# Kernel tuning notes

Measured on AMD Instinct MI355X. Metric: run time of the kernel, lower is better.

Reference implementation:

```python
import jax, jax.numpy as jnp
import numpy as np

N = 50000      # nodes
E = 800000     # edges
CIN = 128
CH = 128
COUT = 64
EPS = 1e-5     # BatchNorm eps


def setup_inputs() -> dict:
    key = jax.random.key(0)
    ks = jax.random.split(key, 16)
    s = 0.1  # weight scale for numerical stability
    return {
        "x": jax.random.normal(ks[0], (N, CIN), jnp.float32),
        "edge_index": jax.random.randint(ks[1], (2, E), 0, N, jnp.int32),
        "edge_weights": jax.random.uniform(ks[2], (E,), jnp.float32),
        "w1": jax.random.normal(ks[3], (CIN, CH), jnp.float32) * s,
        "b1": jnp.zeros((CH,), jnp.float32),
        "bn1_g": jnp.ones((CH,), jnp.float32),
        "bn1_b": jnp.zeros((CH,), jnp.float32),
        "bn1_m": jax.random.normal(ks[4], (CH,), jnp.float32) * 0.1,
        "bn1_v": jax.random.uniform(ks[5], (CH,), jnp.float32) + 0.5,
        "conv_ws": jax.random.normal(ks[6], (2, CH, CH), jnp.float32) * s,
        "conv_bs": jnp.zeros((2, CH), jnp.float32),
        "bns_g": jnp.ones((2, CH), jnp.float32),
        "bns_b": jnp.zeros((2, CH), jnp.float32),
        "bns_m": jax.random.normal(ks[7], (2, CH), jnp.float32) * 0.1,
        "bns_v": jax.random.uniform(ks[8], (2, CH), jnp.float32) + 0.5,
        "lin1_w": jax.random.normal(ks[9], (CH, CH), jnp.float32) * s,
        "lin1_b": jnp.zeros((CH,), jnp.float32),
        "lin2_w": jax.random.normal(ks[10], (CH, COUT), jnp.float32) * s,
        "lin2_b": jnp.zeros((COUT,), jnp.float32),
    }


def _bn(h, g, b, m, v):
    # BatchNorm1d in eval mode: running statistics
    return (h - m) * jax.lax.rsqrt(v + EPS) * g + b


def _gcn(h, w, b, src, dst, norm, n):
    # GCNConv: out[dst] += norm_e * (h @ W)[src]  (self loops already in src/dst)
    h = h @ w
    msg = h[src] * norm[:, None]                 # [E+N, CH]
    return jax.ops.segment_sum(msg, dst, num_segments=n) + b


def reference(x, edge_index, edge_weights, w1, b1, bn1_g, bn1_b, bn1_m, bn1_v,
              conv_ws, conv_bs, bns_g, bns_b, bns_m, bns_v,
              lin1_w, lin1_b, lin2_w, lin2_b):
    n = x.shape[0]
    loop = jnp.arange(n, dtype=edge_index.dtype)
    src = jnp.concatenate([edge_index[0], loop])
    dst = jnp.concatenate([edge_index[1], loop])
    ew = jnp.concatenate([edge_weights, jnp.ones((n,), edge_weights.dtype)])
    # symmetric degree normalization (PyG gcn_norm)
    deg = jax.ops.segment_sum(ew, dst, num_segments=n)
    dis = jnp.where(deg > 0, jax.lax.rsqrt(deg), 0.0)
    norm = dis[src] * ew * dis[dst]

    lrelu = jax.nn.leaky_relu  # slope 0.01, matches F.leaky_relu default
    h = lrelu(_bn(_gcn(x, w1, b1, src, dst, norm, n), bn1_g, bn1_b, bn1_m, bn1_v))
    for i in range(conv_ws.shape[0]):
        h = lrelu(_bn(_gcn(h, conv_ws[i], conv_bs[i], src, dst, norm, n),
                      bns_g[i], bns_b[i], bns_m[i], bns_v[i]) + h)
    h = lrelu(h @ lin1_w + lin1_b)
    # dropout is identity in eval mode
    return h @ lin2_w + lin2_b
```

## Files before the change

kernel.cpp:

```cpp
#include <hip/hip_runtime.h>
#include <hip/hip_bf16.h>


constexpr int   NN    = 50000;
constexpr int   EE    = 800000;
constexpr int   CH    = 128;
constexpr int   SLOTS = 64;
constexpr int   NBUK  = 782;
constexpr int   RCAP  = 2048;
constexpr int   EPB   = 2048;
constexpr float EPS   = 1e-5f;

typedef __attribute__((ext_vector_type(8))) short bf16x8;
typedef __attribute__((ext_vector_type(4))) float f32x4;
typedef unsigned long long u64;
typedef unsigned short u16;

__device__ inline u16 f2bf_rne(float f) {
  unsigned u = __float_as_uint(f);
  unsigned r = u + 0x7fffu + ((u >> 16) & 1u);
  return (u16)(r >> 16);
}
__device__ inline float bf2f(unsigned h16) {
  return __uint_as_float(h16 << 16);
}


__global__ __launch_bounds__(256) void bin_kernel(const int* __restrict__ ei,
                                                  const float* __restrict__ ew,
                                                  unsigned* __restrict__ gcur,
                                                  u64* __restrict__ bins) {
  __shared__ unsigned cnt[NBUK];
  __shared__ unsigned base[NBUK];
  const int tid = threadIdx.x;
  for (int b = tid; b < NBUK; b += 256) cnt[b] = 0;
  __syncthreads();
  const int e0 = blockIdx.x * EPB;
  unsigned pk[8]; u16 bkt[8]; u16 rnk[8]; unsigned char dl[8];
  #pragma unroll
  for (int i = 0; i < 8; i++) {
    int e = e0 + i * 256 + tid;
    if (e < EE) {
      int s = ei[e], d = ei[EE + e];
      float w = ew[e];
      bkt[i] = (u16)(d >> 6);
      dl[i]  = (unsigned char)(d & 63);
      pk[i]  = ((unsigned)f2bf_rne(w) << 16) | (unsigned)s;
      rnk[i] = (u16)atomicAdd(&cnt[bkt[i]], 1u);
    } else bkt[i] = 0xffffu;
  }
  __syncthreads();
  for (int b = tid; b < NBUK; b += 256) {
    unsigned c = cnt[b];
    base[b] = c ? atomicAdd(&gcur[b * 16], c) : 0u;
  }
  __syncthreads();
  #pragma unroll
  for (int i = 0; i < 8; i++) {
    if (bkt[i] == 0xffffu) continue;
    unsigned pos = base[bkt[i]] + rnk[i];
    if (pos < RCAP)
      bins[(size_t)bkt[i] * RCAP + pos] = ((u64)dl[i] << 32) | pk[i];
  }
}


__global__ __launch_bounds__(256) void scatter_kernel(const unsigned* __restrict__ gcur,
                                                      const u64* __restrict__ bins,
                                                      unsigned* __restrict__ ell,
                                                      float* __restrict__ dis) {
  __shared__ unsigned rank[64];
  __shared__ float    wsum[64];
  const int b   = blockIdx.x;
  const int tid = threadIdx.x;
  if (tid < 64) { rank[tid] = 1u; wsum[tid] = 0.f; }
  __syncthreads();
  unsigned cnt = gcur[b * 16];
  if (cnt > RCAP) cnt = RCAP;
  const u64* src = bins + (size_t)b * RCAP;
  for (unsigned i = tid; i < cnt; i += 256) {
    u64 v = src[i];
    unsigned pk = (unsigned)v;
    unsigned dl = (unsigned)(v >> 32);
    unsigned r = atomicAdd(&rank[dl], 1u);
    if (r < SLOTS)
      ell[((size_t)(b * 64 + dl)) * SLOTS + r] = pk;
    atomicAdd(&wsum[dl], bf2f(pk >> 16));
  }
  __syncthreads();
  if (tid < 64) {
    int node = b * 64 + tid;
    if (node < NN) {
      unsigned c = rank[tid];
      if (c > SLOTS) c = SLOTS;
      ell[(size_t)node * SLOTS] = c;
      dis[node] = rsqrtf(1.0f + wsum[tid]);
    }
  }
}

constexpr int NB_WZ = (73728 + 384 + 255) / 256;

__global__ void wswz_kernel(
    const float* __restrict__ w1, const float* __restrict__ bn1_g, const float* __restrict__ bn1_v,
    const float* __restrict__ conv_ws, const float* __restrict__ bns_g, const float* __restrict__ bns_v,
    const float* __restrict__ lin1_w, const float* __restrict__ lin2_w,
    const float* __restrict__ b1, const float* __restrict__ bn1_b, const float* __restrict__ bn1_m,
    const float* __restrict__ conv_bs, const float* __restrict__ bns_b, const float* __restrict__ bns_m,
    u16* __restrict__ w1h, u16* __restrict__ w1l,
    u16* __restrict__ c0h, u16* __restrict__ c0l,
    u16* __restrict__ c1h, u16* __restrict__ c1l,
    u16* __restrict__ l1h, u16* __restrict__ l1l,
    u16* __restrict__ l2h, u16* __restrict__ l2l,
    float* __restrict__ beff)
{
  int idx = blockIdx.x * 256 + threadIdx.x;
  if (idx >= 73728) {
    int r = idx - 73728;
    if (r >= 384) return;
    int l = r >> 7, c = r & 127;
    float bc, gg, bb, mm, vv;
    if (l == 0) { bc = b1[c]; gg = bn1_g[c]; bb = bn1_b[c]; mm = bn1_m[c]; vv = bn1_v[c]; }
    else {
      int o = (l - 1) * 128 + c;
      bc = conv_bs[o]; gg = bns_g[o]; bb = bns_b[o]; mm = bns_m[o]; vv = bns_v[o];
    }
    beff[r] = (bc - mm) * gg * rsqrtf(vv + EPS) + bb;
    return;
  }
  const float* W; const float* g = nullptr; const float* v = nullptr;
  u16 *hi, *lo; int CO = 128; int local;
  if      (idx < 16384) { W = w1;              g = bn1_g;     v = bn1_v;     hi = w1h; lo = w1l; local = idx; }
  else if (idx < 32768) { W = conv_ws;         g = bns_g;     v = bns_v;     hi = c0h; lo = c0l; local = idx - 16384; }
  else if (idx < 49152) { W = conv_ws + 16384; g = bns_g+128; v = bns_v+128; hi = c1h; lo = c1l; local = idx - 32768; }
  else if (idx < 65536) { W = lin1_w;                                        hi = l1h; lo = l1l; local = idx - 49152; }
  else                  { W = lin2_w;                                        hi = l2h; lo = l2l; local = idx - 65536; CO = 64; }
  int k = local / CO, n = local % CO;
  float w = W[local];
  if (g) w *= g[n] * rsqrtf(v[n] + EPS);
  int NCT = CO / 16;
  int kchunk = k >> 5, kin = k & 31, quad = kin >> 3, j = kin & 7;
  int ct = n >> 4, l = (quad << 4) | (n & 15);
  size_t pos = ((size_t)(kchunk * NCT + ct) * 64 + l) * 8 + j;
  u16 h = f2bf_rne(w);
  hi[pos] = h;
  lo[pos] = f2bf_rne(w - bf2f(h));
}

__global__ __launch_bounds__(256) void gemm1_kernel(
    const float* __restrict__ Ain,
    const u16* __restrict__ Whi, const u16* __restrict__ Wlo,
    const float* __restrict__ dis, u16* __restrict__ Cout)
{
  __shared__ float lds[64][CH + 4];
  const int tid  = threadIdx.x;
  const int wave = tid >> 6;
  const int lane = tid & 63;
  const int quad = lane >> 4;
  const int mrow = lane & 15;
  const int row0 = blockIdx.x * 64;

  int arow = row0 + wave * 16 + mrow;
  if (arow >= NN) arow = NN - 1;

  bf16x8 ahi[4], alo[4];
  const float* Ar = Ain + (size_t)arow * CH;
  #pragma unroll
  for (int c = 0; c < 4; c++) {
    int off = c * 32 + quad * 8;
    float4 f0 = *(const float4*)(Ar + off);
    float4 f1 = *(const float4*)(Ar + off + 4);
    float f[8] = {f0.x, f0.y, f0.z, f0.w, f1.x, f1.y, f1.z, f1.w};
    #pragma unroll
    for (int j = 0; j < 8; j++) {
      u16 h = f2bf_rne(f[j]);
      ahi[c][j] = (short)h;
      alo[c][j] = (short)f2bf_rne(f[j] - bf2f(h));
    }
  }

  f32x4 acc[8];
  #pragma unroll
  for (int t = 0; t < 8; t++) acc[t] = (f32x4){0.f, 0.f, 0.f, 0.f};
  #pragma unroll
  for (int c = 0; c < 4; c++) {
    #pragma unroll
    for (int t = 0; t < 8; t++) {
      size_t base = ((size_t)(c * 8 + t) * 64 + lane) * 8;
      bf16x8 bh = *(const bf16x8*)(Whi + base);
      bf16x8 bl = *(const bf16x8*)(Wlo + base);
      acc[t] = __builtin_amdgcn_mfma_f32_16x16x32_bf16(ahi[c], bh, acc[t], 0, 0, 0);
      acc[t] = __builtin_amdgcn_mfma_f32_16x16x32_bf16(alo[c], bh, acc[t], 0, 0, 0);
      acc[t] = __builtin_amdgcn_mfma_f32_16x16x32_bf16(ahi[c], bl, acc[t], 0, 0, 0);
    }
  }

  #pragma unroll
  for (int t = 0; t < 8; t++)
    #pragma unroll
    for (int r = 0; r < 4; r++)
      lds[wave * 16 + quad * 4 + r][t * 16 + mrow] = acc[t][r];
  __syncthreads();

  #pragma unroll
  for (int i = tid; i < 64 * CH / 4; i += 256) {
    int row = (i * 4) / CH;
    int col = (i * 4) % CH;
    int grow = row0 + row;
    if (grow >= NN) continue;
    float rs = dis[grow];
    const float* lp = &lds[row][col];
    u16* cp = (u16*)Cout + (size_t)grow * CH + col;
    unsigned p0 = ((unsigned)f2bf_rne(lp[1] * rs) << 16) | f2bf_rne(lp[0] * rs);
    unsigned p1 = ((unsigned)f2bf_rne(lp[3] * rs) << 16) | f2bf_rne(lp[2] * rs);
    *(uint2*)cp = make_uint2(p0, p1);
  }
}

template<bool RES, bool WH>
__device__ __forceinline__ void gather4_qw(
    const u16* __restrict__ hwin, const unsigned* __restrict__ ell,
    const float* __restrict__ dis, const float* __restrict__ beff,
    const u16* __restrict__ res, u16* __restrict__ hout,
    unsigned* __restrict__ hsbase,
    int nbase, int lane, int sub, int grp)
{
  int nd0 = nbase < NN ? nbase : NN - 1;
  unsigned wcur = ell[(size_t)nd0 * SLOTS + lane];
  for (int r = 0; r < 4; r++) {
    int node = nbase + r;
    int nd = node < NN ? node : NN - 1;
    unsigned myword = wcur;
    if (r < 3) {
      int n2 = node + 1 < NN ? node + 1 : NN - 1;
      wcur = ell[(size_t)n2 * SLOTS + lane];
    }
    int cnt = __shfl((int)myword, 0);
    if (cnt > SLOTS) cnt = SLOTS;
    float a[8] = {0.f, 0.f, 0.f, 0.f, 0.f, 0.f, 0.f, 0.f};
    for (int j = 0; j < cnt; j += 16) {
      unsigned sidx[4]; float wv[4];
      #pragma unroll
      for (int q = 0; q < 4; q++) {
        int jj = j + q * 4 + grp;
        unsigned e = (unsigned)__shfl((int)myword, jj & 63);
        float    w = (jj == 0) ? 1.0f : bf2f(e >> 16);
        unsigned s = (jj == 0) ? (unsigned)nd : (e & 0xffffu);
        if (jj >= cnt) { w = 0.f; s = (unsigned)nd; }
        sidx[q] = s; wv[q] = w;
      }
      uint4 h[4];
      #pragma unroll
      for (int q = 0; q < 4; q++)
        h[q] = *(const uint4*)(hwin + (size_t)sidx[q] * CH + sub * 8);
      #pragma unroll
      for (int q = 0; q < 4; q++) {
        float w = wv[q];
        a[0] = fmaf(w, bf2f(h[q].x & 0xffffu), a[0]); a[1] = fmaf(w, bf2f(h[q].x >> 16), a[1]);
        a[2] = fmaf(w, bf2f(h[q].y & 0xffffu), a[2]); a[3] = fmaf(w, bf2f(h[q].y >> 16), a[3]);
        a[4] = fmaf(w, bf2f(h[q].z & 0xffffu), a[4]); a[5] = fmaf(w, bf2f(h[q].z >> 16), a[5]);
        a[6] = fmaf(w, bf2f(h[q].w & 0xffffu), a[6]); a[7] = fmaf(w, bf2f(h[q].w >> 16), a[7]);
      }
    }
    #pragma unroll
    for (int k = 0; k < 8; k++) {
      a[k] += __shfl_xor(a[k], 16);
      a[k] += __shfl_xor(a[k], 32);
    }
    if (grp == 0) {
      float disd = dis[nd];
      int c = sub * 8;
      float4 be0 = *(const float4*)(beff + c);
      float4 be1 = *(const float4*)(beff + c + 4);
      float y[8];
      y[0] = a[0] * disd + be0.x; y[1] = a[1] * disd + be0.y;
      y[2] = a[2] * disd + be0.z; y[3] = a[3] * disd + be0.w;
      y[4] = a[4] * disd + be1.x; y[5] = a[5] * disd + be1.y;
      y[6] = a[6] * disd + be1.z; y[7] = a[7] * disd + be1.w;
      if constexpr (RES) {
        uint4 rr = *(const uint4*)(res + (size_t)nd * CH + c);
        y[0] += bf2f(rr.x & 0xffffu); y[1] += bf2f(rr.x >> 16);
        y[2] += bf2f(rr.y & 0xffffu); y[3] += bf2f(rr.y >> 16);
        y[4] += bf2f(rr.z & 0xffffu); y[5] += bf2f(rr.z >> 16);
        y[6] += bf2f(rr.w & 0xffffu); y[7] += bf2f(rr.w >> 16);
      }
      #pragma unroll
      for (int k = 0; k < 8; k++) y[k] = y[k] > 0.f ? y[k] : 0.01f * y[k];
      uint4 o;
      o.x = ((unsigned)f2bf_rne(y[1]) << 16) | f2bf_rne(y[0]);
      o.y = ((unsigned)f2bf_rne(y[3]) << 16) | f2bf_rne(y[2]);
      o.z = ((unsigned)f2bf_rne(y[5]) << 16) | f2bf_rne(y[4]);
      o.w = ((unsigned)f2bf_rne(y[7]) << 16) | f2bf_rne(y[6]);
      if constexpr (WH) {
        if (node < NN) *(uint4*)(hout + (size_t)node * CH + c) = o;
      }
      *(uint4*)&hsbase[r * 68 + sub * 4] = o;
    }
  }
}

template<bool RES>
__global__ __launch_bounds__(256, 6) void fuse_kernel(
    const u16* __restrict__ hwin,
    const unsigned* __restrict__ ell, const float* __restrict__ dis,
    const float* __restrict__ beff, const u16* __restrict__ res,
    const u16* __restrict__ Whi, const u16* __restrict__ Wlo,
    u16* __restrict__ hout, u16* __restrict__ hwout)
{
  __shared__ unsigned hs[16][68];
  const int tid  = threadIdx.x;
  const int wave = tid >> 6;
  const int lane = tid & 63;
  const int sub  = lane & 15;
  const int grp  = lane >> 4;
  const int row0 = blockIdx.x * 16;

  gather4_qw<RES, true>(hwin, ell, dis, beff, res, hout,
                        &hs[wave * 4][0], row0 + wave * 4, lane, sub, grp);
  __syncthreads();

  bf16x8 af[4];
  #pragma unroll
  for (int c = 0; c < 4; c++)
    af[c] = *(const bf16x8*)&hs[sub][c * 16 + grp * 4];
  __syncthreads();

  f32x4 acc[2];
  #pragma unroll
  for (int t = 0; t < 2; t++) acc[t] = (f32x4){0.f, 0.f, 0.f, 0.f};
  #pragma unroll
  for (int c = 0; c < 4; c++) {
    #pragma unroll
    for (int t = 0; t < 2; t++) {
      size_t base = ((size_t)(c * 8 + wave * 2 + t) * 64 + lane) * 8;
      bf16x8 bh = *(const bf16x8*)(Whi + base);
      bf16x8 bl = *(const bf16x8*)(Wlo + base);
      acc[t] = __builtin_amdgcn_mfma_f32_16x16x32_bf16(af[c], bh, acc[t], 0, 0, 0);
      acc[t] = __builtin_amdgcn_mfma_f32_16x16x32_bf16(af[c], bl, acc[t], 0, 0, 0);
    }
  }

  u16* hs16 = (u16*)&hs[0][0];
  #pragma unroll
  for (int r = 0; r < 4; r++) {
    int row = grp * 4 + r;
    float rs = dis[row0 + row];
    #pragma unroll
    for (int t = 0; t < 2; t++)
      hs16[row * 136 + wave * 32 + t * 16 + sub] = f2bf_rne(acc[t][r] * rs);
  }
  __syncthreads();
  {
    int row   = tid >> 4;
    int chunk = tid & 15;
    uint4 o = *(const uint4*)(hs16 + row * 136 + chunk * 8);
    *(uint4*)(hwout + (size_t)(row0 + row) * CH + chunk * 8) = o;
  }
}

__global__ __launch_bounds__(256, 6) void fuse_last_kernel(
    const u16* __restrict__ hwin,
    const unsigned* __restrict__ ell, const float* __restrict__ dis,
    const float* __restrict__ beff, const u16* __restrict__ res,
    const u16* __restrict__ l1h, const u16* __restrict__ l1l,
    const float* __restrict__ b1,
    const u16* __restrict__ l2h, const u16* __restrict__ l2l,
    const float* __restrict__ b2, float* __restrict__ out)
{
  __shared__ unsigned hs[16][68];
  __shared__ float    fs[16][132];
  const int tid  = threadIdx.x;
  const int wave = tid >> 6;
  const int lane = tid & 63;
  const int sub  = lane & 15;
  const int grp  = lane >> 4;
  const int row0 = blockIdx.x * 16;

  gather4_qw<true, false>(hwin, ell, dis, beff, res, nullptr,
                          &hs[wave * 4][0], row0 + wave * 4, lane, sub, grp);
  __syncthreads();

  bf16x8 af[4];
  #pragma unroll
  for (int c = 0; c < 4; c++)
    af[c] = *(const bf16x8*)&hs[sub][c * 16 + grp * 4];

  f32x4 acc[2];
  #pragma unroll
  for (int t = 0; t < 2; t++) acc[t] = (f32x4){0.f, 0.f, 0.f, 0.f};
  #pragma unroll
  for (int c = 0; c < 4; c++) {
    #pragma unroll
    for (int t = 0; t < 2; t++) {
      size_t base = ((size_t)(c * 8 + wave * 2 + t) * 64 + lane) * 8;
      bf16x8 bh = *(const bf16x8*)(l1h + base);
      bf16x8 bl = *(const bf16x8*)(l1l + base);
      acc[t] = __builtin_amdgcn_mfma_f32_16x16x32_bf16(af[c], bh, acc[t], 0, 0, 0);
      acc[t] = __builtin_amdgcn_mfma_f32_16x16x32_bf16(af[c], bl, acc[t], 0, 0, 0);
    }
  }
  #pragma unroll
  for (int t = 0; t < 2; t++) {
    int col = wave * 32 + t * 16 + sub;
    float bb = b1[col];
    #pragma unroll
    for (int r = 0; r < 4; r++) {
      float x = acc[t][r] + bb;
      x = x > 0.f ? x : 0.01f * x;
      fs[grp * 4 + r][col] = x;
    }
  }
  __syncthreads();

  f32x4 acc2 = (f32x4){0.f, 0.f, 0.f, 0.f};
  #pragma unroll
  for (int c = 0; c < 4; c++) {
    bf16x8 ahi, alo;
    const float* lp = &fs[sub][c * 32 + grp * 8];
    float4 f0 = *(const float4*)lp;
    float4 f1 = *(const float4*)(lp + 4);
    float f[8] = {f0.x, f0.y, f0.z, f0.w, f1.x, f1.y, f1.z, f1.w};
    #pragma unroll
    for (int j = 0; j < 8; j++) {
      u16 h = f2bf_rne(f[j]);
      ahi[j] = (short)h;
      alo[j] = (short)f2bf_rne(f[j] - bf2f(h));
    }
    size_t base = ((size_t)(c * 4 + wave) * 64 + lane) * 8;
    bf16x8 bh = *(const bf16x8*)(l2h + base);
    bf16x8 bl = *(const bf16x8*)(l2l + base);
    acc2 = __builtin_amdgcn_mfma_f32_16x16x32_bf16(ahi, bh, acc2, 0, 0, 0);
    acc2 = __builtin_amdgcn_mfma_f32_16x16x32_bf16(alo, bh, acc2, 0, 0, 0);
    acc2 = __builtin_amdgcn_mfma_f32_16x16x32_bf16(ahi, bl, acc2, 0, 0, 0);
  }
  {
    float bb = b2[wave * 16 + sub];
    #pragma unroll
    for (int r = 0; r < 4; r++) {
      int grow = row0 + grp * 4 + r;
      if (grow < NN)
        out[(size_t)grow * 64 + wave * 16 + sub] = acc2[r] + bb;
    }
  }
}


extern "C" void kernel_launch(void* const* d_in, const int* in_sizes, int n_in,
                              void* d_out, int out_size, void* d_ws, size_t ws_size,
                              hipStream_t stream) {
  const float* x       = (const float*)d_in[0];
  const int*   ei      = (const int*)  d_in[1];
  const float* ew      = (const float*)d_in[2];
  const float* w1      = (const float*)d_in[3];
  const float* b1      = (const float*)d_in[4];
  const float* bn1_g   = (const float*)d_in[5];
  const float* bn1_b   = (const float*)d_in[6];
  const float* bn1_m   = (const float*)d_in[7];
  const float* bn1_v   = (const float*)d_in[8];
  const float* conv_ws = (const float*)d_in[9];
  const float* conv_bs = (const float*)d_in[10];
  const float* bns_g   = (const float*)d_in[11];
  const float* bns_b   = (const float*)d_in[12];
  const float* bns_m   = (const float*)d_in[13];
  const float* bns_v   = (const float*)d_in[14];
  const float* lin1_w  = (const float*)d_in[15];
  const float* lin1_b  = (const float*)d_in[16];
  const float* lin2_w  = (const float*)d_in[17];
  const float* lin2_b  = (const float*)d_in[18];
  float* out = (float*)d_out;

  size_t off = 0;
  auto alloc = [&](size_t elems) -> void* {
    void* p = (char*)d_ws + off * 4;
    off += (elems + 3) & ~(size_t)3;
    return p;
  };
  unsigned* gcur = (unsigned*)alloc(NBUK * 16);
  u64*      bins = (u64*)     alloc((size_t)NBUK * RCAP * 2);
  unsigned* ell  = (unsigned*)alloc((size_t)NN * SLOTS);
  float*    dis  = (float*)   alloc(NN);
  float*    beff = (float*)   alloc(3 * CH);
  u16*      hwa  = (u16*)     alloc((size_t)NN * CH / 2);
  u16*      hwb  = (u16*)     alloc((size_t)NN * CH / 2);
  u16*      h1   = (u16*)     alloc((size_t)NN * CH / 2);
  u16*      h2   = (u16*)     alloc((size_t)NN * CH / 2);
  u16* w1h = (u16*)alloc(CH * CH / 2); u16* w1l = (u16*)alloc(CH * CH / 2);
  u16* c0h = (u16*)alloc(CH * CH / 2); u16* c0l = (u16*)alloc(CH * CH / 2);
  u16* c1h = (u16*)alloc(CH * CH / 2); u16* c1l = (u16*)alloc(CH * CH / 2);
  u16* l1h = (u16*)alloc(CH * CH / 2); u16* l1l = (u16*)alloc(CH * CH / 2);
  u16* l2h = (u16*)alloc(CH * 64 / 2); u16* l2l = (u16*)alloc(CH * 64 / 2);

  const int nb_bin  = (EE + EPB - 1) / EPB;
  const int nb_gemm = (NN + 63) / 64;
  const int nb_fuse = (NN + 15) / 16;
  dim3 B(256);

  hipMemsetAsync(gcur, 0, NBUK * 16 * sizeof(unsigned), stream);
  bin_kernel    <<<nb_bin, B, 0, stream>>>(ei, ew, gcur, bins);
  scatter_kernel<<<NBUK,   B, 0, stream>>>(gcur, bins, ell, dis);

  wswz_kernel<<<NB_WZ, B, 0, stream>>>(w1, bn1_g, bn1_v, conv_ws, bns_g, bns_v,
      lin1_w, lin2_w, b1, bn1_b, bn1_m, conv_bs, bns_b, bns_m,
      w1h, w1l, c0h, c0l, c1h, c1l, l1h, l1l, l2h, l2l, beff);

  gemm1_kernel<<<nb_gemm, B, 0, stream>>>(x, w1h, w1l, dis, hwa);

  fuse_kernel<false><<<nb_fuse, B, 0, stream>>>(hwa, ell, dis, beff, nullptr,
      c0h, c0l, h1, hwb);

  fuse_kernel<true><<<nb_fuse, B, 0, stream>>>(hwb, ell, dis, beff + CH, h1,
      c1h, c1l, h2, hwa);

  fuse_last_kernel<<<nb_fuse, B, 0, stream>>>(hwa, ell, dis, beff + 2 * CH, h2,
      l1h, l1l, lin1_b, l2h, l2l, lin2_b, out);
}
```

Before: 302.2 us.

## Merge binning with weight swizzle and scatter with first GEMM

```diff
diff --git a/kernel.cpp b/kernel.cpp
--- a/kernel.cpp
+++ b/kernel.cpp
@@ -9,6 +9,8 @@
 constexpr int   NBUK  = 782;
 constexpr int   RCAP  = 2048;
 constexpr int   EPB   = 2048;
+constexpr int   NB_BIN = (EE + EPB - 1) / EPB;
+constexpr int   NB_WZ  = (73728 + 384 + 255) / 256;
 constexpr float EPS   = 1e-5f;
 
 typedef __attribute__((ext_vector_type(8))) short bf16x8;
@@ -26,82 +28,9 @@
 }
 
 
-__global__ __launch_bounds__(256) void bin_kernel(const int* __restrict__ ei,
-                                                  const float* __restrict__ ew,
-                                                  unsigned* __restrict__ gcur,
-                                                  u64* __restrict__ bins) {
-  __shared__ unsigned cnt[NBUK];
-  __shared__ unsigned base[NBUK];
-  const int tid = threadIdx.x;
-  for (int b = tid; b < NBUK; b += 256) cnt[b] = 0;
-  __syncthreads();
-  const int e0 = blockIdx.x * EPB;
-  unsigned pk[8]; u16 bkt[8]; u16 rnk[8]; unsigned char dl[8];
-  #pragma unroll
-  for (int i = 0; i < 8; i++) {
-    int e = e0 + i * 256 + tid;
-    if (e < EE) {
-      int s = ei[e], d = ei[EE + e];
-      float w = ew[e];
-      bkt[i] = (u16)(d >> 6);
-      dl[i]  = (unsigned char)(d & 63);
-      pk[i]  = ((unsigned)f2bf_rne(w) << 16) | (unsigned)s;
-      rnk[i] = (u16)atomicAdd(&cnt[bkt[i]], 1u);
-    } else bkt[i] = 0xffffu;
-  }
-  __syncthreads();
-  for (int b = tid; b < NBUK; b += 256) {
-    unsigned c = cnt[b];
-    base[b] = c ? atomicAdd(&gcur[b * 16], c) : 0u;
-  }
-  __syncthreads();
-  #pragma unroll
-  for (int i = 0; i < 8; i++) {
-    if (bkt[i] == 0xffffu) continue;
-    unsigned pos = base[bkt[i]] + rnk[i];
-    if (pos < RCAP)
-      bins[(size_t)bkt[i] * RCAP + pos] = ((u64)dl[i] << 32) | pk[i];
-  }
-}
-
-
-__global__ __launch_bounds__(256) void scatter_kernel(const unsigned* __restrict__ gcur,
-                                                      const u64* __restrict__ bins,
-                                                      unsigned* __restrict__ ell,
-                                                      float* __restrict__ dis) {
-  __shared__ unsigned rank[64];
-  __shared__ float    wsum[64];
-  const int b   = blockIdx.x;
-  const int tid = threadIdx.x;
-  if (tid < 64) { rank[tid] = 1u; wsum[tid] = 0.f; }
-  __syncthreads();
-  unsigned cnt = gcur[b * 16];
-  if (cnt > RCAP) cnt = RCAP;
-  const u64* src = bins + (size_t)b * RCAP;
-  for (unsigned i = tid; i < cnt; i += 256) {
-    u64 v = src[i];
-    unsigned pk = (unsigned)v;
-    unsigned dl = (unsigned)(v >> 32);
-    unsigned r = atomicAdd(&rank[dl], 1u);
-    if (r < SLOTS)
-      ell[((size_t)(b * 64 + dl)) * SLOTS + r] = pk;
-    atomicAdd(&wsum[dl], bf2f(pk >> 16));
-  }
-  __syncthreads();
-  if (tid < 64) {
-    int node = b * 64 + tid;
-    if (node < NN) {
-      unsigned c = rank[tid];
-      if (c > SLOTS) c = SLOTS;
-      ell[(size_t)node * SLOTS] = c;
-      dis[node] = rsqrtf(1.0f + wsum[tid]);
-    }
-  }
-}
-
-constexpr int NB_WZ = (73728 + 384 + 255) / 256;
-
-__global__ void wswz_kernel(
+__global__ __launch_bounds__(256) void binw_kernel(
+    const int* __restrict__ ei, const float* __restrict__ ew,
+    unsigned* __restrict__ gcur, u64* __restrict__ bins,
     const float* __restrict__ w1, const float* __restrict__ bn1_g, const float* __restrict__ bn1_v,
     const float* __restrict__ conv_ws, const float* __restrict__ bns_g, const float* __restrict__ bns_v,
     const float* __restrict__ lin1_w, const float* __restrict__ lin2_w,
@@ -114,51 +43,122 @@
     u16* __restrict__ l2h, u16* __restrict__ l2l,
     float* __restrict__ beff)
 {
-  int idx = blockIdx.x * 256 + threadIdx.x;
-  if (idx >= 73728) {
-    int r = idx - 73728;
-    if (r >= 384) return;
-    int l = r >> 7, c = r & 127;
-    float bc, gg, bb, mm, vv;
-    if (l == 0) { bc = b1[c]; gg = bn1_g[c]; bb = bn1_b[c]; mm = bn1_m[c]; vv = bn1_v[c]; }
-    else {
-      int o = (l - 1) * 128 + c;
-      bc = conv_bs[o]; gg = bns_g[o]; bb = bns_b[o]; mm = bns_m[o]; vv = bns_v[o];
-    }
-    beff[r] = (bc - mm) * gg * rsqrtf(vv + EPS) + bb;
+  const int tid = threadIdx.x;
+  if (blockIdx.x >= NB_BIN) {
+    int idx = (blockIdx.x - NB_BIN) * 256 + tid;
+    if (idx >= 73728) {
+      int r = idx - 73728;
+      if (r >= 384) return;
+      int l = r >> 7, c = r & 127;
+      float bc, gg, bb, mm, vv;
+      if (l == 0) { bc = b1[c]; gg = bn1_g[c]; bb = bn1_b[c]; mm = bn1_m[c]; vv = bn1_v[c]; }
+      else {
+        int o = (l - 1) * 128 + c;
+        bc = conv_bs[o]; gg = bns_g[o]; bb = bns_b[o]; mm = bns_m[o]; vv = bns_v[o];
+      }
+      beff[r] = (bc - mm) * gg * rsqrtf(vv + EPS) + bb;
+      return;
+    }
+    const float* W; const float* g = nullptr; const float* v = nullptr;
+    u16 *hi, *lo; int CO = 128; int local;
+    if      (idx < 16384) { W = w1;              g = bn1_g;     v = bn1_v;     hi = w1h; lo = w1l; local = idx; }
+    else if (idx < 32768) { W = conv_ws;         g = bns_g;     v = bns_v;     hi = c0h; lo = c0l; local = idx - 16384; }
+    else if (idx < 49152) { W = conv_ws + 16384; g = bns_g+128; v = bns_v+128; hi = c1h; lo = c1l; local = idx - 32768; }
+    else if (idx < 65536) { W = lin1_w;                                        hi = l1h; lo = l1l; local = idx - 49152; }
+    else                  { W = lin2_w;                                        hi = l2h; lo = l2l; local = idx - 65536; CO = 64; }
+    int k = local / CO, n = local % CO;
+    float w = W[local];
+    if (g) w *= g[n] * rsqrtf(v[n] + EPS);
+    int NCT = CO / 16;
+    int kchunk = k >> 5, kin = k & 31, quad = kin >> 3, j = kin & 7;
+    int ct = n >> 4, l = (quad << 4) | (n & 15);
+    size_t pos = ((size_t)(kchunk * NCT + ct) * 64 + l) * 8 + j;
+    u16 h = f2bf_rne(w);
+    hi[pos] = h;
+    lo[pos] = f2bf_rne(w - bf2f(h));
     return;
   }
-  const float* W; const float* g = nullptr; const float* v = nullptr;
-  u16 *hi, *lo; int CO = 128; int local;
-  if      (idx < 16384) { W = w1;              g = bn1_g;     v = bn1_v;     hi = w1h; lo = w1l; local = idx; }
-  else if (idx < 32768) { W = conv_ws;         g = bns_g;     v = bns_v;     hi = c0h; lo = c0l; local = idx - 16384; }
-  else if (idx < 49152) { W = conv_ws + 16384; g = bns_g+128; v = bns_v+128; hi = c1h; lo = c1l; local = idx - 32768; }
-  else if (idx < 65536) { W = lin1_w;                                        hi = l1h; lo = l1l; local = idx - 49152; }
-  else                  { W = lin2_w;                                        hi = l2h; lo = l2l; local = idx - 65536; CO = 64; }
-  int k = local / CO, n = local % CO;
-  float w = W[local];
-  if (g) w *= g[n] * rsqrtf(v[n] + EPS);
-  int NCT = CO / 16;
-  int kchunk = k >> 5, kin = k & 31, quad = kin >> 3, j = kin & 7;
-  int ct = n >> 4, l = (quad << 4) | (n & 15);
-  size_t pos = ((size_t)(kchunk * NCT + ct) * 64 + l) * 8 + j;
-  u16 h = f2bf_rne(w);
-  hi[pos] = h;
-  lo[pos] = f2bf_rne(w - bf2f(h));
-}
-
-__global__ __launch_bounds__(256) void gemm1_kernel(
+  __shared__ unsigned cnt[NBUK];
+  __shared__ unsigned base[NBUK];
+  for (int b = tid; b < NBUK; b += 256) cnt[b] = 0;
+  __syncthreads();
+  const int e0 = blockIdx.x * EPB;
+  unsigned pk[8]; u16 bkt[8]; u16 rnk[8]; unsigned char dl[8];
+  #pragma unroll
+  for (int i = 0; i < 8; i++) {
+    int e = e0 + i * 256 + tid;
+    if (e < EE) {
+      int s = ei[e], d = ei[EE + e];
+      float w = ew[e];
+      bkt[i] = (u16)(d >> 6);
+      dl[i]  = (unsigned char)(d & 63);
+      pk[i]  = ((unsigned)f2bf_rne(w) << 16) | (unsigned)s;
+      rnk[i] = (u16)atomicAdd(&cnt[bkt[i]], 1u);
+    } else bkt[i] = 0xffffu;
+  }
+  __syncthreads();
+  for (int b = tid; b < NBUK; b += 256) {
+    unsigned c = cnt[b];
+    base[b] = c ? atomicAdd(&gcur[b * 16], c) : 0u;
+  }
+  __syncthreads();
+  #pragma unroll
+  for (int i = 0; i < 8; i++) {
+    if (bkt[i] == 0xffffu) continue;
+    unsigned pos = base[bkt[i]] + rnk[i];
+    if (pos < RCAP)
+      bins[(size_t)bkt[i] * RCAP + pos] = ((u64)dl[i] << 32) | pk[i];
+  }
+}
+
+
+__global__ __launch_bounds__(256) void scatgemm_kernel(
+    const unsigned* __restrict__ gcur, const u64* __restrict__ bins,
+    unsigned* __restrict__ ell, float* __restrict__ dis,
     const float* __restrict__ Ain,
     const u16* __restrict__ Whi, const u16* __restrict__ Wlo,
-    const float* __restrict__ dis, u16* __restrict__ Cout)
+    u16* __restrict__ Cout)
 {
-  __shared__ float lds[64][CH + 4];
-  const int tid  = threadIdx.x;
+  __shared__ unsigned rank[64];
+  __shared__ float    wsum[64];
+  __shared__ float    disl[64];
+  __shared__ float    lds[64][CH + 4];
+  const int b   = blockIdx.x;
+  const int tid = threadIdx.x;
+
+  if (tid < 64) { rank[tid] = 1u; wsum[tid] = 0.f; }
+  __syncthreads();
+  unsigned cnt = gcur[b * 16];
+  if (cnt > RCAP) cnt = RCAP;
+  const u64* src = bins + (size_t)b * RCAP;
+  for (unsigned i = tid; i < cnt; i += 256) {
+    u64 v = src[i];
+    unsigned pk = (unsigned)v;
+    unsigned dl = (unsigned)(v >> 32);
+    unsigned r = atomicAdd(&rank[dl], 1u);
+    if (r < SLOTS)
+      ell[((size_t)(b * 64 + dl)) * SLOTS + r] = pk;
+    atomicAdd(&wsum[dl], bf2f(pk >> 16));
+  }
+  __syncthreads();
+  if (tid < 64) {
+    int node = b * 64 + tid;
+    float d = rsqrtf(1.0f + wsum[tid]);
+    disl[tid] = d;
+    if (node < NN) {
+      unsigned c = rank[tid];
+      if (c > SLOTS) c = SLOTS;
+      ell[(size_t)node * SLOTS] = c;
+      dis[node] = d;
+    }
+  }
+  __syncthreads();
+
   const int wave = tid >> 6;
   const int lane = tid & 63;
   const int quad = lane >> 4;
   const int mrow = lane & 15;
-  const int row0 = blockIdx.x * 64;
+  const int row0 = b * 64;
 
   int arow = row0 + wave * 16 + mrow;
   if (arow >= NN) arow = NN - 1;
@@ -208,7 +208,7 @@
     int col = (i * 4) % CH;
     int grow = row0 + row;
     if (grow >= NN) continue;
-    float rs = dis[grow];
+    float rs = disl[row];
     const float* lp = &lds[row][col];
     u16* cp = (u16*)Cout + (size_t)grow * CH + col;
     unsigned p0 = ((unsigned)f2bf_rne(lp[1] * rs) << 16) | f2bf_rne(lp[0] * rs);
@@ -490,20 +490,17 @@
   u16* l1h = (u16*)alloc(CH * CH / 2); u16* l1l = (u16*)alloc(CH * CH / 2);
   u16* l2h = (u16*)alloc(CH * 64 / 2); u16* l2l = (u16*)alloc(CH * 64 / 2);
 
-  const int nb_bin  = (EE + EPB - 1) / EPB;
-  const int nb_gemm = (NN + 63) / 64;
   const int nb_fuse = (NN + 15) / 16;
   dim3 B(256);
 
   hipMemsetAsync(gcur, 0, NBUK * 16 * sizeof(unsigned), stream);
-  bin_kernel    <<<nb_bin, B, 0, stream>>>(ei, ew, gcur, bins);
-  scatter_kernel<<<NBUK,   B, 0, stream>>>(gcur, bins, ell, dis);
-
-  wswz_kernel<<<NB_WZ, B, 0, stream>>>(w1, bn1_g, bn1_v, conv_ws, bns_g, bns_v,
-      lin1_w, lin2_w, b1, bn1_b, bn1_m, conv_bs, bns_b, bns_m,
+
+  binw_kernel<<<NB_BIN + NB_WZ, B, 0, stream>>>(ei, ew, gcur, bins,
+      w1, bn1_g, bn1_v, conv_ws, bns_g, bns_v, lin1_w, lin2_w,
+      b1, bn1_b, bn1_m, conv_bs, bns_b, bns_m,
       w1h, w1l, c0h, c0l, c1h, c1l, l1h, l1l, l2h, l2l, beff);
 
-  gemm1_kernel<<<nb_gemm, B, 0, stream>>>(x, w1h, w1l, dis, hwa);
+  scatgemm_kernel<<<NBUK, B, 0, stream>>>(gcur, bins, ell, dis, x, w1h, w1l, hwa);
 
   fuse_kernel<false><<<nb_fuse, B, 0, stream>>>(hwa, ell, dis, beff, nullptr,
       c0h, c0l, h1, hwb);
```

After: 296.8 us. Within noise of the previous version (-1.8%).
